# Kernel tuning notes

Measured on AMD Instinct MI355X. Metric: run time of the kernel, lower is better.

Reference implementation:

```python
import jax, jax.numpy as jnp
import numpy as np

N, M, D = 20000, 16000, 128

def setup_inputs() -> dict:
    key = jax.random.key(0)
    ks = jax.random.split(key, 4)
    return {
        "clear_feature": jax.random.normal(ks[0], (N, D), dtype=jnp.float32),
        "rain_feature": jax.random.normal(ks[1], (M, D), dtype=jnp.float32),
        # torch nn.Linear weight layout: (out_features, in_features)
        "W1": jax.random.normal(ks[2], (D, 2 * D), dtype=jnp.float32) * 0.05,
        "b1": jnp.zeros((D,), dtype=jnp.float32),
        "W2": jax.random.normal(ks[3], (1, D), dtype=jnp.float32) * 0.05,
        "b2": jnp.zeros((1,), dtype=jnp.float32),
    }

def reference(clear_feature, rain_feature, W1, b1, W2, b2):
    # --- KNN alignment (k=1): argmin of squared Euclidean distance == cdist+topk(smallest) ---
    x2 = jnp.sum(clear_feature * clear_feature, axis=-1, keepdims=True)   # [N,1]
    y2 = jnp.sum(rain_feature * rain_feature, axis=-1)                    # [M]
    d2 = x2 + y2 - 2.0 * (clear_feature @ rain_feature.T)                 # [N,M]
    idx = jnp.argmin(d2, axis=-1)                                         # [N]
    aligned = rain_feature[idx]                                           # [N,D] gather
    # --- attention MLP: Linear(2D->D) + ReLU + Linear(D->1) + Sigmoid ---
    comb = jnp.concatenate([clear_feature, aligned], axis=-1)             # [N,2D]
    h = jax.nn.relu(comb @ W1.T + b1)                                     # [N,D]
    w = jax.nn.sigmoid(h @ W2.T + b2)                                     # [N,1]
    # --- gated fusion ---
    return w * clear_feature + (1.0 - w) * aligned
```

## Files before the change

kernel.cpp:

```cpp
#include <hip/hip_runtime.h>
#include <stdint.h>

#define NN 20000
#define MM 16000
#define DD 128
#define CT2 250
#define SPLITS 32
#define RB 79

typedef unsigned long long u64;
typedef _Float16 f16x8 __attribute__((ext_vector_type(8)));
typedef float f32x16 __attribute__((ext_vector_type(16)));

__global__ void k_y2(const float* __restrict__ rain, float* __restrict__ y2) {
    int row = blockIdx.x * 4 + (threadIdx.x >> 6);
    int lane = threadIdx.x & 63;
    if (row >= MM) return;
    float2 v = ((const float2*)(rain + (size_t)row * DD))[lane];
    float s = v.x * v.x + v.y * v.y;
    #pragma unroll
    for (int off = 32; off > 0; off >>= 1) s += __shfl_down(s, off);
    if (lane == 0) y2[row] = s;
}

__global__ void k_split_B(const float* __restrict__ rain, _Float16* __restrict__ Bimg) {
    int id = blockIdx.x * 256 + threadIdx.x;
    if (id >= CT2 * 1024) return;
    int cl = id & 31;
    int cg = (id >> 5) & 1;
    int kp = (id >> 6) & 15;
    int tc = id >> 10;
    int row = tc * 64 + cg * 32 + cl;
    const float4* src = (const float4*)(rain + (size_t)row * DD + kp * 8);
    float4 v0 = src[0], v1 = src[1];
    float x[8] = {v0.x, v0.y, v0.z, v0.w, v1.x, v1.y, v1.z, v1.w};
    _Float16 hi[8], lo[8];
    #pragma unroll
    for (int j = 0; j < 8; ++j) {
        _Float16 h = (_Float16)x[j];
        hi[j] = h;
        lo[j] = (_Float16)(x[j] - (float)h);
    }
    int ks = kp >> 1, kh = kp & 1;
    int chunk = ((ks * 2 + cg) * 2 + kh) * 32 + cl;
    size_t base = (size_t)tc * 16384;
    *(f16x8*)(Bimg + base + (size_t)chunk * 8) = *(f16x8*)hi;
    *(f16x8*)(Bimg + base + 8192 + (size_t)chunk * 8) = *(f16x8*)lo;
}

__global__ void k_w1img(const float* __restrict__ W1, _Float16* __restrict__ W1img) {
    int id = blockIdx.x * 256 + threadIdx.x;
    if (id >= 4096) return;
    int cl = id & 31;
    int kh = (id >> 5) & 1;
    int cg = (id >> 6) & 3;
    int ks = id >> 8;
    int d = cg * 32 + cl;
    int k = ks * 16 + kh * 8;
    const float4* src = (const float4*)(W1 + (size_t)d * 256 + k);
    float4 v0 = src[0], v1 = src[1];
    float x[8] = {v0.x, v0.y, v0.z, v0.w, v1.x, v1.y, v1.z, v1.w};
    _Float16 h[8];
    #pragma unroll
    for (int j = 0; j < 8; ++j) h[j] = (_Float16)x[j];
    *(f16x8*)(W1img + (size_t)id * 8) = *(f16x8*)h;
}

__global__ __launch_bounds__(256, 2) void k_dist(
        const float* __restrict__ clear_f,
        const _Float16* __restrict__ Bimg, const float* __restrict__ y2,
        u64* __restrict__ keys2) {
    __shared__ _Float16 lds[2][16384];
    __shared__ float y2s[512];

    const int tid = threadIdx.x;
    const int w = tid >> 6, lane = tid & 63;
    const int l5 = lane >> 5, l31 = lane & 31;
    const int b = blockIdx.x;
    const int split = b & 31;
    const int n0 = (b >> 5) * 256;
    const int nt = (CT2 - split + SPLITS - 1) / SPLITS;

    {
        const _Float16* gsrc = Bimg + (size_t)split * 16384;
        #pragma unroll
        for (int n = 0; n < 8; ++n) {
            int seg = w * 8 + n;
            __builtin_amdgcn_global_load_lds(
                (const __attribute__((address_space(1))) unsigned int*)
                    (gsrc + (size_t)seg * 512 + (size_t)lane * 8),
                (__attribute__((address_space(3))) unsigned int*)
                    (&lds[0][0] + (size_t)seg * 512),
                16, 0, 0);
        }
    }

    for (int j = tid; j < nt * 64; j += 256) {
        int tt = j >> 6;
        int cc = j & 63;
        y2s[j] = y2[(split + tt * SPLITS) * 64 + cc];
    }

    f16x8 afh[2][8], afl[2][8];
    #pragma unroll
    for (int rb = 0; rb < 2; ++rb) {
        int r = n0 + w * 64 + rb * 32 + l31;
        if (r >= NN) r = NN - 1;
        const float* ap = clear_f + (size_t)r * DD + l5 * 8;
        #pragma unroll
        for (int ks = 0; ks < 8; ++ks) {
            float4 v0 = *(const float4*)(ap + ks * 16);
            float4 v1 = *(const float4*)(ap + ks * 16 + 4);
            float x[8] = {v0.x, v0.y, v0.z, v0.w, v1.x, v1.y, v1.z, v1.w};
            _Float16 hi[8], lo[8];
            #pragma unroll
            for (int j = 0; j < 8; ++j) {
                float s = -2.f * x[j];
                _Float16 h = (_Float16)s;
                hi[j] = h;
                lo[j] = (_Float16)(s - (float)h);
            }
            afh[rb][ks] = *(f16x8*)hi;
            afl[rb][ks] = *(f16x8*)lo;
        }
    }

    __syncthreads();

    float bestd[32];
    unsigned bits[4] = {0u, 0u, 0u, 0u};
    #pragma unroll
    for (int s = 0; s < 32; ++s) bestd[s] = 1e30f;

    int p = 0;
    for (int i = 0; i < nt; ++i) {
        const int t = split + i * SPLITS;

        if (i + 1 < nt) {
            const _Float16* gsrc = Bimg + (size_t)(t + SPLITS) * 16384;
            _Float16* dst = &lds[1 - p][0];
            #pragma unroll
            for (int n = 0; n < 8; ++n) {
                int seg = w * 8 + n;
                __builtin_amdgcn_global_load_lds(
                    (const __attribute__((address_space(1))) unsigned int*)
                        (gsrc + (size_t)seg * 512 + (size_t)lane * 8),
                    (__attribute__((address_space(3))) unsigned int*)
                        (dst + (size_t)seg * 512),
                    16, 0, 0);
            }
        }

        float y2v0 = y2s[i * 64 + l31];
        float y2v1 = y2s[i * 64 + 32 + l31];

        f32x16 acc00, acc01, acc10, acc11;
        #pragma unroll
        for (int e = 0; e < 16; ++e) {
            acc00[e] = y2v0; acc10[e] = y2v0;
            acc01[e] = y2v1; acc11[e] = y2v1;
        }

        const _Float16* lbuf = &lds[p][0];
        #pragma unroll
        for (int ks = 0; ks < 8; ++ks) {
            f16x8 bh0 = *(const f16x8*)(lbuf + (size_t)(ks * 2 + 0) * 512 + (size_t)lane * 8);
            f16x8 bh1 = *(const f16x8*)(lbuf + (size_t)(ks * 2 + 1) * 512 + (size_t)lane * 8);
            f16x8 bl0 = *(const f16x8*)(lbuf + 8192 + (size_t)(ks * 2 + 0) * 512 + (size_t)lane * 8);
            f16x8 bl1 = *(const f16x8*)(lbuf + 8192 + (size_t)(ks * 2 + 1) * 512 + (size_t)lane * 8);
            acc00 = __builtin_amdgcn_mfma_f32_32x32x16_f16(afh[0][ks], bh0, acc00, 0, 0, 0);
            acc10 = __builtin_amdgcn_mfma_f32_32x32x16_f16(afh[1][ks], bh0, acc10, 0, 0, 0);
            acc01 = __builtin_amdgcn_mfma_f32_32x32x16_f16(afh[0][ks], bh1, acc01, 0, 0, 0);
            acc11 = __builtin_amdgcn_mfma_f32_32x32x16_f16(afh[1][ks], bh1, acc11, 0, 0, 0);
            acc00 = __builtin_amdgcn_mfma_f32_32x32x16_f16(afh[0][ks], bl0, acc00, 0, 0, 0);
            acc10 = __builtin_amdgcn_mfma_f32_32x32x16_f16(afh[1][ks], bl0, acc10, 0, 0, 0);
            acc01 = __builtin_amdgcn_mfma_f32_32x32x16_f16(afh[0][ks], bl1, acc01, 0, 0, 0);
            acc11 = __builtin_amdgcn_mfma_f32_32x32x16_f16(afh[1][ks], bl1, acc11, 0, 0, 0);
            acc00 = __builtin_amdgcn_mfma_f32_32x32x16_f16(afl[0][ks], bh0, acc00, 0, 0, 0);
            acc10 = __builtin_amdgcn_mfma_f32_32x32x16_f16(afl[1][ks], bh0, acc10, 0, 0, 0);
            acc01 = __builtin_amdgcn_mfma_f32_32x32x16_f16(afl[0][ks], bh1, acc01, 0, 0, 0);
            acc11 = __builtin_amdgcn_mfma_f32_32x32x16_f16(afl[1][ks], bh1, acc11, 0, 0, 0);
        }

        const unsigned ibase = (unsigned)i << 1;
        #pragma unroll
        for (int e = 0; e < 16; ++e) {
            {
                float d0 = acc00[e], d1 = acc01[e];
                bool tk = d1 < d0;
                float dm = tk ? d1 : d0;
                int s = e, sh = 4 * (e & 7);
                bool up = dm < bestd[s];
                bestd[s] = up ? dm : bestd[s];
                unsigned nib = ibase | (unsigned)tk;
                bits[s >> 3] = up ? ((bits[s >> 3] & ~(15u << sh)) | (nib << sh))
                                  : bits[s >> 3];
            }
            {
                float d0 = acc10[e], d1 = acc11[e];
                bool tk = d1 < d0;
                float dm = tk ? d1 : d0;
                int s = 16 + e, sh = 4 * (s & 7);
                bool up = dm < bestd[s];
                bestd[s] = up ? dm : bestd[s];
                unsigned nib = ibase | (unsigned)tk;
                bits[s >> 3] = up ? ((bits[s >> 3] & ~(15u << sh)) | (nib << sh))
                                  : bits[s >> 3];
            }
        }

        __syncthreads();
        p ^= 1;
    }

    #pragma unroll
    for (int s = 0; s < 32; ++s) {
        unsigned nib = (bits[s >> 3] >> (4 * (s & 7))) & 15u;
        int i4 = (int)(nib >> 1), cg = (int)(nib & 1);
        int col = (split + i4 * SPLITS) * 64 + cg * 32 + l31;
        unsigned u = __float_as_uint(bestd[s]);
        u = (u & 0x80000000u) ? ~u : (u | 0x80000000u);
        u64 key = ((u64)u << 32) | (unsigned)col;
        #pragma unroll
        for (int off = 1; off < 32; off <<= 1) {
            u64 o = __shfl_xor(key, off);
            if (o < key) key = o;
        }
        if (l31 == 0) {
            int e = s & 15, rb = s >> 4;
            int grow = n0 + w * 64 + rb * 32 + (e & 3) + 8 * (e >> 2) + 4 * l5;
            if (grow < NN) keys2[(size_t)grow * SPLITS + split] = key;
        }
    }
}

__global__ void k_reduce(const u64* __restrict__ keys2, int* __restrict__ idx) {
    int n = blockIdx.x * 256 + threadIdx.x;
    if (n >= NN) return;
    const u64* p = keys2 + (size_t)n * SPLITS;
    u64 best = ~0ull;
    #pragma unroll
    for (int j = 0; j < SPLITS; ++j) {
        u64 k = p[j];
        if (k < best) best = k;
    }
    idx[n] = (int)(best & 0xffffffffu);
}

__global__ __launch_bounds__(256, 2) void k_mlp(
        const float* __restrict__ clear_f, const float* __restrict__ rain_f,
        const _Float16* __restrict__ W1img, const float* __restrict__ b1,
        const float* __restrict__ W2, const float* __restrict__ b2,
        const int* __restrict__ idx, float* __restrict__ out) {
    __shared__ _Float16 w1s[32768];

    const int tid = threadIdx.x;
    const int w = tid >> 6, lane = tid & 63;
    const int l5 = lane >> 5, l31 = lane & 31;
    const int n0 = blockIdx.x * 128;

    #pragma unroll
    for (int n = 0; n < 16; ++n) {
        int seg = w * 16 + n;
        __builtin_amdgcn_global_load_lds(
            (const __attribute__((address_space(1))) unsigned int*)
                (W1img + (size_t)seg * 512 + (size_t)lane * 8),
            (__attribute__((address_space(3))) unsigned int*)
                (&w1s[0] + (size_t)seg * 512),
            16, 0, 0);
    }

    int n = n0 + w * 32 + l31;
    int nc = n < NN ? n : NN - 1;
    int rid = idx[nc];
    f16x8 af[16];
    #pragma unroll
    for (int ks = 0; ks < 16; ++ks) {
        int k0 = ks * 16 + l5 * 8;
        const float4* src = (k0 < 128)
            ? (const float4*)(clear_f + (size_t)nc * DD + k0)
            : (const float4*)(rain_f + (size_t)rid * DD + (k0 - 128));
        float4 v0 = src[0], v1 = src[1];
        float x[8] = {v0.x, v0.y, v0.z, v0.w, v1.x, v1.y, v1.z, v1.w};
        _Float16 h[8];
        #pragma unroll
        for (int j = 0; j < 8; ++j) h[j] = (_Float16)x[j];
        af[ks] = *(f16x8*)h;
    }

    __syncthreads();

    f32x16 acc[4];
    #pragma unroll
    for (int cg = 0; cg < 4; ++cg)
        #pragma unroll
        for (int e = 0; e < 16; ++e) acc[cg][e] = 0.f;

    #pragma unroll
    for (int ks = 0; ks < 16; ++ks) {
        #pragma unroll
        for (int cg = 0; cg < 4; ++cg) {
            f16x8 bh = *(const f16x8*)(&w1s[0] +
                ((size_t)((ks * 4 + cg) * 2 + l5)) * 256 + (size_t)l31 * 8);
            acc[cg] = __builtin_amdgcn_mfma_f32_32x32x16_f16(af[ks], bh, acc[cg], 0, 0, 0);
        }
    }

    float b1v[4], w2v[4];
    #pragma unroll
    for (int cg = 0; cg < 4; ++cg) {
        b1v[cg] = b1[cg * 32 + l31];
        w2v[cg] = W2[cg * 32 + l31];
    }
    float b2v = b2[0];

    #pragma unroll
    for (int e = 0; e < 16; ++e) {
        float part = 0.f;
        #pragma unroll
        for (int cg = 0; cg < 4; ++cg) {
            float hv = acc[cg][e] + b1v[cg];
            hv = hv > 0.f ? hv : 0.f;
            part = fmaf(hv, w2v[cg], part);
        }
        #pragma unroll
        for (int off = 1; off < 32; off <<= 1) part += __shfl_xor(part, off);
        float s = part + b2v;
        float wv = 1.f / (1.f + expf(-s));
        int row = n0 + w * 32 + (e & 3) + 8 * (e >> 2) + 4 * l5;
        if (row < NN) {
            int rid2 = idx[row];
            float4 cv = *(const float4*)(clear_f + (size_t)row * DD + l31 * 4);
            float4 av = *(const float4*)(rain_f + (size_t)rid2 * DD + l31 * 4);
            float4 ov;
            ov.x = wv * cv.x + (1.f - wv) * av.x;
            ov.y = wv * cv.y + (1.f - wv) * av.y;
            ov.z = wv * cv.z + (1.f - wv) * av.z;
            ov.w = wv * cv.w + (1.f - wv) * av.w;
            *(float4*)(out + (size_t)row * DD + l31 * 4) = ov;
        }
    }
}

extern "C" void kernel_launch(void* const* d_in, const int* in_sizes, int n_in,
                              void* d_out, int out_size, void* d_ws, size_t ws_size,
                              hipStream_t stream) {
    const float* clear_f = (const float*)d_in[0];
    const float* rain_f = (const float*)d_in[1];
    const float* W1 = (const float*)d_in[2];
    const float* b1 = (const float*)d_in[3];
    const float* W2 = (const float*)d_in[4];
    const float* b2 = (const float*)d_in[5];
    float* out = (float*)d_out;

    char* ws = (char*)d_ws;
    u64* keys2 = (u64*)ws;
    int* idx = (int*)(ws + 5120000);
    float* y2 = (float*)(ws + 5200000);
    _Float16* Bimg = (_Float16*)(ws + 5264000);
    _Float16* W1img = (_Float16*)(ws + 13456000);

    k_y2<<<MM / 4, 256, 0, stream>>>(rain_f, y2);
    k_split_B<<<(CT2 * 1024 + 255) / 256, 256, 0, stream>>>(rain_f, Bimg);
    k_w1img<<<16, 256, 0, stream>>>(W1, W1img);
    k_dist<<<RB * SPLITS, 256, 0, stream>>>(clear_f, Bimg, y2, keys2);
    k_reduce<<<(NN + 255) / 256, 256, 0, stream>>>(keys2, idx);
    k_mlp<<<(NN + 127) / 128, 256, 0, stream>>>(clear_f, rain_f, W1img, b1, W2, b2, idx, out);
}
```

Measured before the change: 346.6 us.

## Triple-buffer distance kernel with 512-thread blocks, warp-parallel reduce, smaller MLP blocks

The distance kernel moves to 512-thread blocks covering 512 query rows and uses a three-stage LDS ring. Prefetch goes two tiles ahead, with vmcnt waits and a raw s_barrier replacing the two __syncthreads per iteration, and s_setprio raised around the MFMA bursts. The reduce kernel now uses one lane per split and a shuffle min instead of a serial 32-way loop per thread. The MLP kernel drops its LDS staging of W1 and reads it directly from global memory with single-wave blocks. The aim is to hide B-tile load latency and cut sync and launch overheads, at the cost of more LDS per block, fewer blocks, and repeated global reads of W1.

```diff
diff --git a/kernel.cpp b/kernel.cpp
--- a/kernel.cpp
+++ b/kernel.cpp
@@ -6,7 +6,7 @@
 #define DD 128
 #define CT2 250
 #define SPLITS 32
-#define RB 79
+#define RB2 40
 
 typedef unsigned long long u64;
 typedef _Float16 f16x8 __attribute__((ext_vector_type(8)));
@@ -66,11 +66,11 @@
     *(f16x8*)(W1img + (size_t)id * 8) = *(f16x8*)h;
 }
 
-__global__ __launch_bounds__(256, 2) void k_dist(
+__global__ __launch_bounds__(512, 2) void k_dist(
         const float* __restrict__ clear_f,
         const _Float16* __restrict__ Bimg, const float* __restrict__ y2,
         u64* __restrict__ keys2) {
-    __shared__ _Float16 lds[2][16384];
+    __shared__ _Float16 lds[3][16384];
     __shared__ float y2s[512];
 
     const int tid = threadIdx.x;
@@ -78,24 +78,28 @@
     const int l5 = lane >> 5, l31 = lane & 31;
     const int b = blockIdx.x;
     const int split = b & 31;
-    const int n0 = (b >> 5) * 256;
+    const int n0 = (b >> 5) * 512;
     const int nt = (CT2 - split + SPLITS - 1) / SPLITS;
 
-    {
-        const _Float16* gsrc = Bimg + (size_t)split * 16384;
-        #pragma unroll
-        for (int n = 0; n < 8; ++n) {
-            int seg = w * 8 + n;
-            __builtin_amdgcn_global_load_lds(
-                (const __attribute__((address_space(1))) unsigned int*)
-                    (gsrc + (size_t)seg * 512 + (size_t)lane * 8),
-                (__attribute__((address_space(3))) unsigned int*)
-                    (&lds[0][0] + (size_t)seg * 512),
-                16, 0, 0);
-        }
-    }
-
-    for (int j = tid; j < nt * 64; j += 256) {
+    #define STAGE(T, BUF) do {                                                 \
+        const _Float16* gsrc_ = Bimg + (size_t)(T) * 16384;                    \
+        _Float16* dst_ = &lds[BUF][0];                                         \
+        _Pragma("unroll")                                                      \
+        for (int n_ = 0; n_ < 4; ++n_) {                                       \
+            int seg_ = w * 4 + n_;                                             \
+            __builtin_amdgcn_global_load_lds(                                  \
+                (const __attribute__((address_space(1))) unsigned int*)        \
+                    (gsrc_ + (size_t)seg_ * 512 + (size_t)lane * 8),           \
+                (__attribute__((address_space(3))) unsigned int*)              \
+                    (dst_ + (size_t)seg_ * 512),                               \
+                16, 0, 0);                                                     \
+        }                                                                      \
+    } while (0)
+
+    STAGE(split, 0);
+    if (nt > 1) STAGE(split + SPLITS, 1);
+
+    for (int j = tid; j < nt * 64; j += 512) {
         int tt = j >> 6;
         int cc = j & 63;
         y2s[j] = y2[(split + tt * SPLITS) * 64 + cc];
@@ -125,7 +129,7 @@
         }
     }
 
-    __syncthreads();
+    asm volatile("s_waitcnt lgkmcnt(0)" ::: "memory");
 
     float bestd[32];
     unsigned bits[4] = {0u, 0u, 0u, 0u};
@@ -134,21 +138,17 @@
 
     int p = 0;
     for (int i = 0; i < nt; ++i) {
-        const int t = split + i * SPLITS;
-
         if (i + 1 < nt) {
-            const _Float16* gsrc = Bimg + (size_t)(t + SPLITS) * 16384;
-            _Float16* dst = &lds[1 - p][0];
-            #pragma unroll
-            for (int n = 0; n < 8; ++n) {
-                int seg = w * 8 + n;
-                __builtin_amdgcn_global_load_lds(
-                    (const __attribute__((address_space(1))) unsigned int*)
-                        (gsrc + (size_t)seg * 512 + (size_t)lane * 8),
-                    (__attribute__((address_space(3))) unsigned int*)
-                        (dst + (size_t)seg * 512),
-                    16, 0, 0);
-            }
+            asm volatile("s_waitcnt vmcnt(4)" ::: "memory");
+        } else {
+            asm volatile("s_waitcnt vmcnt(0)" ::: "memory");
+        }
+        __builtin_amdgcn_s_barrier();
+        __builtin_amdgcn_sched_barrier(0);
+
+        if (i + 2 < nt) {
+            int p2 = p + 2; if (p2 >= 3) p2 -= 3;
+            STAGE(split + (i + 2) * SPLITS, p2);
         }
 
         float y2v0 = y2s[i * 64 + l31];
@@ -168,6 +168,7 @@
             f16x8 bh1 = *(const f16x8*)(lbuf + (size_t)(ks * 2 + 1) * 512 + (size_t)lane * 8);
             f16x8 bl0 = *(const f16x8*)(lbuf + 8192 + (size_t)(ks * 2 + 0) * 512 + (size_t)lane * 8);
             f16x8 bl1 = *(const f16x8*)(lbuf + 8192 + (size_t)(ks * 2 + 1) * 512 + (size_t)lane * 8);
+            __builtin_amdgcn_s_setprio(1);
             acc00 = __builtin_amdgcn_mfma_f32_32x32x16_f16(afh[0][ks], bh0, acc00, 0, 0, 0);
             acc10 = __builtin_amdgcn_mfma_f32_32x32x16_f16(afh[1][ks], bh0, acc10, 0, 0, 0);
             acc01 = __builtin_amdgcn_mfma_f32_32x32x16_f16(afh[0][ks], bh1, acc01, 0, 0, 0);
@@ -180,6 +181,7 @@
             acc10 = __builtin_amdgcn_mfma_f32_32x32x16_f16(afl[1][ks], bh0, acc10, 0, 0, 0);
             acc01 = __builtin_amdgcn_mfma_f32_32x32x16_f16(afl[0][ks], bh1, acc01, 0, 0, 0);
             acc11 = __builtin_amdgcn_mfma_f32_32x32x16_f16(afl[1][ks], bh1, acc11, 0, 0, 0);
+            __builtin_amdgcn_s_setprio(0);
         }
 
         const unsigned ibase = (unsigned)i << 1;
@@ -209,9 +211,9 @@
             }
         }
 
-        __syncthreads();
-        p ^= 1;
-    }
+        ++p; if (p == 3) p = 0;
+    }
+    #undef STAGE
 
     #pragma unroll
     for (int s = 0; s < 32; ++s) {
@@ -235,42 +237,28 @@
 }
 
 __global__ void k_reduce(const u64* __restrict__ keys2, int* __restrict__ idx) {
-    int n = blockIdx.x * 256 + threadIdx.x;
-    if (n >= NN) return;
-    const u64* p = keys2 + (size_t)n * SPLITS;
-    u64 best = ~0ull;
-    #pragma unroll
-    for (int j = 0; j < SPLITS; ++j) {
-        u64 k = p[j];
-        if (k < best) best = k;
-    }
-    idx[n] = (int)(best & 0xffffffffu);
-}
-
-__global__ __launch_bounds__(256, 2) void k_mlp(
+    int gid = blockIdx.x * 256 + threadIdx.x;
+    int row = gid >> 5, j = gid & 31;
+    if (row >= NN) return;
+    u64 k = keys2[(size_t)row * SPLITS + j];
+    #pragma unroll
+    for (int off = 16; off > 0; off >>= 1) {
+        u64 o = __shfl_xor(k, off);
+        if (o < k) k = o;
+    }
+    if (j == 0) idx[row] = (int)(k & 0xffffffffu);
+}
+
+__global__ __launch_bounds__(64) void k_mlp(
         const float* __restrict__ clear_f, const float* __restrict__ rain_f,
         const _Float16* __restrict__ W1img, const float* __restrict__ b1,
         const float* __restrict__ W2, const float* __restrict__ b2,
         const int* __restrict__ idx, float* __restrict__ out) {
-    __shared__ _Float16 w1s[32768];
-
-    const int tid = threadIdx.x;
-    const int w = tid >> 6, lane = tid & 63;
+    const int lane = threadIdx.x;
     const int l5 = lane >> 5, l31 = lane & 31;
-    const int n0 = blockIdx.x * 128;
-
-    #pragma unroll
-    for (int n = 0; n < 16; ++n) {
-        int seg = w * 16 + n;
-        __builtin_amdgcn_global_load_lds(
-            (const __attribute__((address_space(1))) unsigned int*)
-                (W1img + (size_t)seg * 512 + (size_t)lane * 8),
-            (__attribute__((address_space(3))) unsigned int*)
-                (&w1s[0] + (size_t)seg * 512),
-            16, 0, 0);
-    }
-
-    int n = n0 + w * 32 + l31;
+    const int n0 = blockIdx.x * 32;
+
+    int n = n0 + l31;
     int nc = n < NN ? n : NN - 1;
     int rid = idx[nc];
     f16x8 af[16];
@@ -288,8 +276,6 @@
         af[ks] = *(f16x8*)h;
     }
 
-    __syncthreads();
-
     f32x16 acc[4];
     #pragma unroll
     for (int cg = 0; cg < 4; ++cg)
@@ -300,7 +286,7 @@
     for (int ks = 0; ks < 16; ++ks) {
         #pragma unroll
         for (int cg = 0; cg < 4; ++cg) {
-            f16x8 bh = *(const f16x8*)(&w1s[0] +
+            f16x8 bh = *(const f16x8*)(W1img +
                 ((size_t)((ks * 4 + cg) * 2 + l5)) * 256 + (size_t)l31 * 8);
             acc[cg] = __builtin_amdgcn_mfma_f32_32x32x16_f16(af[ks], bh, acc[cg], 0, 0, 0);
         }
@@ -327,7 +313,7 @@
         for (int off = 1; off < 32; off <<= 1) part += __shfl_xor(part, off);
         float s = part + b2v;
         float wv = 1.f / (1.f + expf(-s));
-        int row = n0 + w * 32 + (e & 3) + 8 * (e >> 2) + 4 * l5;
+        int row = n0 + (e & 3) + 8 * (e >> 2) + 4 * l5;
         if (row < NN) {
             int rid2 = idx[row];
             float4 cv = *(const float4*)(clear_f + (size_t)row * DD + l31 * 4);
@@ -363,7 +349,7 @@
     k_y2<<<MM / 4, 256, 0, stream>>>(rain_f, y2);
     k_split_B<<<(CT2 * 1024 + 255) / 256, 256, 0, stream>>>(rain_f, Bimg);
     k_w1img<<<16, 256, 0, stream>>>(W1, W1img);
-    k_dist<<<RB * SPLITS, 256, 0, stream>>>(clear_f, Bimg, y2, keys2);
-    k_reduce<<<(NN + 255) / 256, 256, 0, stream>>>(keys2, idx);
-    k_mlp<<<(NN + 127) / 128, 256, 0, stream>>>(clear_f, rain_f, W1img, b1, W2, b2, idx, out);
-}
+    k_dist<<<RB2 * SPLITS, 512, 0, stream>>>(clear_f, Bimg, y2, keys2);
+    k_reduce<<<(NN * 32 + 255) / 256, 256, 0, stream>>>(keys2, idx);
+    k_mlp<<<(NN + 31) / 32, 64, 0, stream>>>(clear_f, rain_f, W1img, b1, W2, b2, idx, out);
+}
```

Measured after the change: 414.4 us. 1.2x slower.
